# Optimization experiments

Measured on AMD Instinct MI355X. Metric: run time of the kernel, lower is better.

The kernel has to match this reference:

```python
import jax, jax.numpy as jnp
import numpy as np

B, T, D, H = 2, 2048, 1024, 16
HD = D // H  # head_dim = 64


def setup_inputs() -> dict:
    key = jax.random.key(0)
    ks = jax.random.split(key, 5)
    s = 0.02
    return {
        "x": jax.random.normal(ks[0], (B, T, D), dtype=jnp.float32),
        "Wqkv": jax.random.normal(ks[1], (3 * D, D), dtype=jnp.float32) * s,
        "bqkv": jax.random.normal(ks[2], (3 * D,), dtype=jnp.float32) * s,
        "Wproj": jax.random.normal(ks[3], (D, D), dtype=jnp.float32) * s,
        "bproj": jax.random.normal(ks[4], (D,), dtype=jnp.float32) * s,
    }


def reference(x, Wqkv, bqkv, Wproj, bproj):
    b, t, d = x.shape
    qkv = x @ Wqkv.T + bqkv                      # [B,T,3D]
    q, k, v = jnp.split(qkv, 3, axis=-1)
    # [B,T,D] -> [B,H,T,HD]
    def to_heads(u):
        return u.reshape(b, t, H, HD).transpose(0, 2, 1, 3)
    q, k, v = to_heads(q), to_heads(k), to_heads(v)
    scale = 1.0 / jnp.sqrt(jnp.float32(HD))
    attn = jnp.einsum("bhqd,bhkd->bhqk", q, k) * scale   # [B,H,T,T]
    causal = jnp.tril(jnp.ones((t, t), dtype=bool))
    attn = jnp.where(causal[None, None, :, :], attn, -jnp.inf)
    attn = jax.nn.softmax(attn, axis=-1)
    scores = jnp.einsum("bhqk,bhkd->bhqd", attn, v)       # [B,H,T,HD]
    scores = scores.transpose(0, 2, 1, 3).reshape(b, t, d)
    return scores @ Wproj.T + bproj
```

## Files before the change

kernel.cpp:

```cpp
#include <hip/hip_runtime.h>

typedef __bf16 bf16_8 __attribute__((ext_vector_type(8)));
typedef __bf16 bf16_4 __attribute__((ext_vector_type(4)));
typedef float  f32_4  __attribute__((ext_vector_type(4)));
typedef short  s16x4  __attribute__((ext_vector_type(4)));

typedef __attribute__((address_space(1))) const void* as1_cvp;
typedef __attribute__((address_space(3))) void*       as3_vp;

__device__ __forceinline__ void load16_to_lds(const void* g, void* l) {
    __builtin_amdgcn_global_load_lds((as1_cvp)g, (as3_vp)l, 16, 0, 0);
}

__device__ __forceinline__ f32_4 mfma16x16x16(bf16_4 a, bf16_4 b, f32_4 c) {
#if __has_builtin(__builtin_amdgcn_mfma_f32_16x16x16_bf16)
    return __builtin_amdgcn_mfma_f32_16x16x16_bf16(a, b, c, 0, 0, 0);
#else
    return __builtin_amdgcn_mfma_f32_16x16x16bf16_1k(
        __builtin_bit_cast(s16x4, a), __builtin_bit_cast(s16x4, b), c, 0, 0, 0);
#endif
}

__global__ __launch_bounds__(256) void cvt_all(
    const float* __restrict__ a, const float* __restrict__ b,
    const float* __restrict__ c, __bf16* __restrict__ out,
    int na4, int nb4, int nc4)
{
    int i = blockIdx.x * 256 + threadIdx.x;
    if (i >= na4 + nb4 + nc4) return;
    float4 f;
    if (i < na4)            f = ((const float4*)a)[i];
    else if (i < na4 + nb4) f = ((const float4*)b)[i - na4];
    else                    f = ((const float4*)c)[i - na4 - nb4];
    bf16_4 v = { (__bf16)f.x, (__bf16)f.y, (__bf16)f.z, (__bf16)f.w };
    ((bf16_4*)out)[i] = v;
}

#define BM 128

template<int OUT_BF16, int BN_, int QKV>
__global__ __launch_bounds__(256) void gemm_bt(
    const __bf16* __restrict__ A,
    const __bf16* __restrict__ B,
    const float*  __restrict__ bias,
    __bf16* __restrict__ Cb, float* __restrict__ Cf,
    __bf16* __restrict__ Vtb,
    int M, int N, int K, int ldc)
{
    constexpr int NT   = BN_ / 32;
    constexpr int CSTR = BN_ + (OUT_BF16 ? 8 : 4);
    __shared__ __align__(16) char smem[34816];
    __bf16* As = (__bf16*)smem;
    __bf16* Bs = (__bf16*)(smem + 16384);

    const int tid  = threadIdx.x;
    const int wave = tid >> 6;
    const int lane = tid & 63;
    const int wm = wave >> 1, wn = wave & 1;
    const int quad = lane >> 4, l16 = lane & 15;
    const int bm = blockIdx.y * BM, bn = blockIdx.x * BN_;

    const int r0 = tid >> 2;
    const int cf = ((tid & 3) ^ (r0 & 3)) * 8;

    f32_4 acc[4][NT];
    #pragma unroll
    for (int i = 0; i < 4; ++i)
        #pragma unroll
        for (int j = 0; j < NT; ++j)
            acc[i][j] = f32_4{0.f, 0.f, 0.f, 0.f};

    const int NIT = K >> 5;

    {
        #pragma unroll
        for (int p = 0; p < 2; ++p)
            load16_to_lds(A + (size_t)(bm + p * 64 + r0) * K + cf,
                          &As[(p * 64 + wave * 16) * 32]);
        #pragma unroll
        for (int p = 0; p < BN_ / 64; ++p)
            load16_to_lds(B + (size_t)(bn + p * 64 + r0) * K + cf,
                          &Bs[(p * 64 + wave * 16) * 32]);
    }

    for (int j = 0; j < NIT; ++j) {
        const int cur = j & 1, nxt = cur ^ 1;
        __syncthreads();

        if (j + 1 < NIT) {
            const int k0 = (j + 1) * 32;
            #pragma unroll
            for (int p = 0; p < 2; ++p)
                load16_to_lds(A + (size_t)(bm + p * 64 + r0) * K + k0 + cf,
                              &As[nxt * 4096 + (p * 64 + wave * 16) * 32]);
            #pragma unroll
            for (int p = 0; p < BN_ / 64; ++p)
                load16_to_lds(B + (size_t)(bn + p * 64 + r0) * K + k0 + cf,
                              &Bs[nxt * (BN_ * 32) + (p * 64 + wave * 16) * 32]);
        }

        const int sl = ((quad ^ (l16 & 3)) << 3);
        bf16_8 af[4], bfr[NT];
        #pragma unroll
        for (int mt = 0; mt < 4; ++mt)
            af[mt] = *(const bf16_8*)&As[cur * 4096 + (wm * 64 + mt * 16 + l16) * 32 + sl];
        #pragma unroll
        for (int nt = 0; nt < NT; ++nt)
            bfr[nt] = *(const bf16_8*)&Bs[cur * (BN_ * 32) + (wn * (BN_/2) + nt * 16 + l16) * 32 + sl];
        #pragma unroll
        for (int mt = 0; mt < 4; ++mt)
            #pragma unroll
            for (int nt = 0; nt < NT; ++nt)
                acc[mt][nt] = __builtin_amdgcn_mfma_f32_16x16x32_bf16(
                    af[mt], bfr[nt], acc[mt][nt], 0, 0, 0);
    }

    __syncthreads();

    if (QKV && bn >= 2048) {
        constexpr int VSTR = 136;
        __bf16* Cs = (__bf16*)smem;
        const int b_ = bm >> 11;
        const int t0 = bm & 2047;
        #pragma unroll
        for (int nt = 0; nt < NT; ++nt) {
            int col = wn * (BN_/2) + nt * 16 + l16;
            float bv = bias ? bias[bn + col] : 0.f;
            #pragma unroll
            for (int mt = 0; mt < 4; ++mt) {
                bf16_4 ov;
                #pragma unroll
                for (int r = 0; r < 4; ++r)
                    ov[r] = (__bf16)(acc[mt][nt][r] + bv);
                *(bf16_4*)&Cs[col * VSTR + wm * 64 + mt * 16 + quad * 4] = ov;
            }
        }
        __syncthreads();
        const int rr = tid >> 1, hh = tid & 1;
        #pragma unroll
        for (int c = 0; c < 8; ++c) {
            bf16_8 v = *(const bf16_8*)&Cs[rr * VSTR + (hh * 8 + c) * 8];
            *(bf16_8*)(Vtb + ((size_t)b_ * 1024 + (bn - 2048) + rr) * 2048
                       + t0 + (hh * 8 + c) * 8) = v;
        }
        return;
    }

    if (OUT_BF16) {
        __bf16* Cs = (__bf16*)smem;
        #pragma unroll
        for (int mt = 0; mt < 4; ++mt)
            #pragma unroll
            for (int nt = 0; nt < NT; ++nt) {
                int col = wn * (BN_/2) + nt * 16 + l16;
                float bv = bias ? bias[bn + col] : 0.f;
                #pragma unroll
                for (int r = 0; r < 4; ++r)
                    Cs[(wm * 64 + mt * 16 + quad * 4 + r) * CSTR + col] =
                        (__bf16)(acc[mt][nt][r] + bv);
            }
        __syncthreads();
        const int rr = tid >> 4, cc = (tid & 15) * 8;
        #pragma unroll
        for (int p = 0; p < 8; ++p) {
            int row = p * 16 + rr;
            bf16_8 v = *(const bf16_8*)&Cs[row * CSTR + cc];
            *(bf16_8*)(Cb + (size_t)(bm + row) * ldc + bn + cc) = v;
        }
    } else {
        float* Cs = (float*)smem;
        #pragma unroll
        for (int mt = 0; mt < 4; ++mt)
            #pragma unroll
            for (int nt = 0; nt < NT; ++nt) {
                int col = wn * (BN_/2) + nt * 16 + l16;
                float bv = bias ? bias[bn + col] : 0.f;
                #pragma unroll
                for (int r = 0; r < 4; ++r)
                    Cs[(wm * 64 + mt * 16 + quad * 4 + r) * CSTR + col] =
                        acc[mt][nt][r] + bv;
            }
        __syncthreads();
        const int rr = tid >> 4, cc = (tid & 15) * 4;
        #pragma unroll
        for (int p = 0; p < 8; ++p) {
            int row = p * 16 + rr;
            float4 v = *(const float4*)&Cs[row * CSTR + cc];
            *(float4*)(Cf + (size_t)(bm + row) * ldc + bn + cc) = v;
        }
    }
}

__global__ __launch_bounds__(512, 4) void attn_kernel(
    const __bf16* __restrict__ qk, const __bf16* __restrict__ vt,
    __bf16* __restrict__ out)
{
    constexpr int T = 2048;
    __shared__ __align__(16) char pool[35328];
    __bf16* Ks = (__bf16*)pool;
    __bf16* Vt = (__bf16*)(pool + 16384);
    float*  Om = (float*)pool;
    float*  Lm = (float*)(pool + 34816);

    const int tid  = threadIdx.x;
    const int wave = tid >> 6;
    const int lane = tid & 63;
    const int wg = wave >> 2, wq = wave & 3;
    const int quad = lane >> 4, l16 = lane & 15;

    const int fid  = blockIdx.x;
    const int xcd  = fid & 7;
    const int half = fid >> 8;
    const int w    = (fid >> 3) & 31;
    const int qt   = half ? (7 - (w >> 2)) : ((w >> 2) + 8);
    const int bh   = xcd * 4 + (w & 3);
    const int b = bh >> 4, h = bh & 15;
    const int jmax = 2 * qt + 1;

    const size_t rowbase = (size_t)b * T;
    const __bf16* Kbase = qk + 1024 + h * 64;
    const __bf16* Vbase = vt + (size_t)bh * 64 * 2048;

    const int srow = tid >> 3;
    const int sch  = tid & 7;
    const int schf = sch ^ (srow & 7);

    bf16_8 aq[2][2];
    #pragma unroll
    for (int mt = 0; mt < 2; ++mt) {
        const __bf16* qrow =
            qk + (rowbase + qt * 128 + wq * 32 + mt * 16 + l16) * 2048 + h * 64;
        aq[mt][0] = *(const bf16_8*)(qrow + quad * 8);
        aq[mt][1] = *(const bf16_8*)(qrow + 32 + quad * 8);
        #pragma unroll
        for (int u = 0; u < 8; ++u) {
            aq[mt][0][u] = (__bf16)((float)aq[mt][0][u] * 0.125f);
            aq[mt][1][u] = (__bf16)((float)aq[mt][1][u] * 0.125f);
        }
    }

    load16_to_lds(Kbase + (rowbase + srow) * 2048 + schf * 8, &Ks[wave * 512]);
    load16_to_lds(Vbase + (size_t)srow * 2048 + schf * 8,     &Vt[wave * 512]);

    float l_i[2] = {0.f, 0.f};
    f32_4 O[2][4];
    #pragma unroll
    for (int mt = 0; mt < 2; ++mt)
        #pragma unroll
        for (int dt = 0; dt < 4; ++dt) O[mt][dt] = f32_4{0.f, 0.f, 0.f, 0.f};

    for (int j = 0; j <= jmax; ++j) {
        const int cur = j & 1, nxt = cur ^ 1;
        __syncthreads();

        if (j < jmax) {
            const int jn = j + 1;
            load16_to_lds(Kbase + (rowbase + jn * 64 + srow) * 2048 + schf * 8,
                          &Ks[nxt * 4096 + wave * 512]);
            load16_to_lds(Vbase + (size_t)srow * 2048 + jn * 64 + schf * 8,
                          &Vt[nxt * 4096 + wave * 512]);
        }

        f32_4 S[2][2];
        #pragma unroll
        for (int nt = 0; nt < 2; ++nt) {
            int rk = wg * 32 + nt * 16 + l16;
            int rx = rk & 7;
            bf16_8 kb0 = *(const bf16_8*)&Ks[cur * 4096 + rk * 64 + ((quad ^ rx) << 3)];
            bf16_8 kb1 = *(const bf16_8*)&Ks[cur * 4096 + rk * 64 + (((quad + 4) ^ rx) << 3)];
            #pragma unroll
            for (int mt = 0; mt < 2; ++mt) {
                f32_4 zz = {0.f, 0.f, 0.f, 0.f};
                zz = __builtin_amdgcn_mfma_f32_16x16x32_bf16(kb0, aq[mt][0], zz, 0, 0, 0);
                zz = __builtin_amdgcn_mfma_f32_16x16x32_bf16(kb1, aq[mt][1], zz, 0, 0, 0);
                S[mt][nt] = zz;
            }
        }

        const bool diag = (j >= 2 * qt);
        bf16_4 bp[2][2];
        #pragma unroll
        for (int mt = 0; mt < 2; ++mt) {
            int qg = qt * 128 + wq * 32 + mt * 16 + l16;
            #pragma unroll
            for (int nt = 0; nt < 2; ++nt) {
                #pragma unroll
                for (int rr = 0; rr < 4; ++rr) {
                    float p = __expf(S[mt][nt][rr]);
                    if (diag) {
                        int key = j * 64 + wg * 32 + nt * 16 + quad * 4 + rr;
                        if (key > qg) p = 0.f;
                    }
                    l_i[mt] += p;
                    bp[mt][nt][rr] = (__bf16)p;
                }
            }
        }

        #pragma unroll
        for (int dt = 0; dt < 4; ++dt) {
            int d = dt * 16 + l16;
            int dsw = d & 7;
            #pragma unroll
            for (int nt = 0; nt < 2; ++nt) {
                int chv = (wg * 4 + nt * 2 + (quad >> 1)) ^ dsw;
                bf16_4 vaf = *(const bf16_4*)&Vt[cur * 4096 + d * 64 + chv * 8 + (quad & 1) * 4];
                #pragma unroll
                for (int mt = 0; mt < 2; ++mt)
                    O[mt][dt] = mfma16x16x16(vaf, bp[mt][nt], O[mt][dt]);
            }
        }
    }

    float lw[2];
    #pragma unroll
    for (int mt = 0; mt < 2; ++mt) {
        float v = l_i[mt];
        v += __shfl_xor(v, 16, 64);
        v += __shfl_xor(v, 32, 64);
        lw[mt] = v;
    }
    __syncthreads();
    if (wg == 1) {
        #pragma unroll
        for (int mt = 0; mt < 2; ++mt) {
            #pragma unroll
            for (int dt = 0; dt < 4; ++dt)
                *(f32_4*)&Om[(wq * 32 + mt * 16 + l16) * 68 + dt * 16 + quad * 4] = O[mt][dt];
            if (quad == 0) Lm[wq * 32 + mt * 16 + l16] = lw[mt];
        }
    }
    __syncthreads();
    if (wg == 0) {
        #pragma unroll
        for (int mt = 0; mt < 2; ++mt) {
            float inv = 1.f / (lw[mt] + Lm[wq * 32 + mt * 16 + l16]);
            int q = qt * 128 + wq * 32 + mt * 16 + l16;
            #pragma unroll
            for (int dt = 0; dt < 4; ++dt) {
                f32_4 o2 = *(const f32_4*)&Om[(wq * 32 + mt * 16 + l16) * 68 + dt * 16 + quad * 4];
                bf16_4 ov;
                #pragma unroll
                for (int rr = 0; rr < 4; ++rr)
                    ov[rr] = (__bf16)((O[mt][dt][rr] + o2[rr]) * inv);
                *(bf16_4*)(out + (rowbase + q) * 1024 + h * 64 + dt * 16 + quad * 4) = ov;
            }
        }
    }
}

extern "C" void kernel_launch(void* const* d_in, const int* in_sizes, int n_in,
                              void* d_out, int out_size, void* d_ws, size_t ws_size,
                              hipStream_t stream)
{
    constexpr int Bc = 2, Tc = 2048, Dc = 1024;
    constexpr int M  = Bc * Tc;
    constexpr int N1 = 3 * Dc;

    const float* x     = (const float*)d_in[0];
    const float* Wqkv  = (const float*)d_in[1];
    const float* bqkv  = (const float*)d_in[2];
    const float* Wproj = (const float*)d_in[3];
    const float* bproj = (const float*)d_in[4];
    float* outp = (float*)d_out;

    __bf16* xb     = (__bf16*)d_ws;
    __bf16* wqkvb  = xb     + (size_t)M * Dc;
    __bf16* wprojb = wqkvb  + (size_t)N1 * Dc;
    __bf16* qkb    = wprojb + (size_t)Dc * Dc;
    __bf16* vtb    = qkb    + (size_t)M * 2048;
    __bf16* attnb  = vtb    + (size_t)Bc * 1024 * 2048;

    {
        int na4 = M * Dc / 4, nb4 = N1 * Dc / 4, nc4 = Dc * Dc / 4;
        int n4 = na4 + nb4 + nc4;
        cvt_all<<<(n4 + 255) / 256, 256, 0, stream>>>(x, Wqkv, Wproj, xb, na4, nb4, nc4);
    }

    gemm_bt<1, 128, 1><<<dim3(N1 / 128, M / BM), 256, 0, stream>>>(
        xb, wqkvb, bqkv, qkb, nullptr, vtb, M, N1, Dc, 2048);

    attn_kernel<<<dim3(512), 512, 0, stream>>>(qkb, vtb, attnb);

    gemm_bt<0, 64, 0><<<dim3(Dc / 64, M / BM), 256, 0, stream>>>(
        attnb, wprojb, bproj, nullptr, outp, nullptr, M, Dc, Dc, Dc);
}
```

Baseline: 170.6 us.

## Enlarge attention KV tiles, give each block two balanced query tiles

The attention kernel now loads 128-key K/V tiles per iteration and each wave handles 64 query rows across 4 key groups. Each block processes a pair of query tiles (z+8 and 7-z) in sequence, which balances causal work, and the grid is halved to 256 blocks. The cross-wave reduction becomes a two-stage LDS reduce with a swizzled layout. The GEMM LDS swizzle pattern is also changed to reduce bank conflicts. Risks: LDS doubles to about 66KB, occupancy drops (launch bounds go from 4 to 2), and the accumulators use more registers.

```diff
diff --git a/kernel.cpp b/kernel.cpp
--- a/kernel.cpp
+++ b/kernel.cpp
@@ -61,7 +61,7 @@
     const int bm = blockIdx.y * BM, bn = blockIdx.x * BN_;
 
     const int r0 = tid >> 2;
-    const int cf = ((tid & 3) ^ (r0 & 3)) * 8;
+    const int cf = ((tid & 3) ^ ((tid >> 3) & 3)) * 8;
 
     f32_4 acc[4][NT];
     #pragma unroll
@@ -99,7 +99,7 @@
                               &Bs[nxt * (BN_ * 32) + (p * 64 + wave * 16) * 32]);
         }
 
-        const int sl = ((quad ^ (l16 & 3)) << 3);
+        const int sl = ((quad ^ ((l16 >> 1) & 3)) << 3);
         bf16_8 af[4], bfr[NT];
         #pragma unroll
         for (int mt = 0; mt < 4; ++mt)
@@ -191,161 +191,199 @@
     }
 }
 
-__global__ __launch_bounds__(512, 4) void attn_kernel(
+__global__ __launch_bounds__(512, 2) void attn_kernel(
     const __bf16* __restrict__ qk, const __bf16* __restrict__ vt,
     __bf16* __restrict__ out)
 {
     constexpr int T = 2048;
-    __shared__ __align__(16) char pool[35328];
+    __shared__ __align__(16) char pool[67584];
     __bf16* Ks = (__bf16*)pool;
-    __bf16* Vt = (__bf16*)(pool + 16384);
+    __bf16* Vt = (__bf16*)(pool + 32768);
     float*  Om = (float*)pool;
-    float*  Lm = (float*)(pool + 34816);
+    float*  Lm = (float*)(pool + 65536);
 
     const int tid  = threadIdx.x;
     const int wave = tid >> 6;
     const int lane = tid & 63;
-    const int wg = wave >> 2, wq = wave & 3;
+    const int wq = wave >> 2;
+    const int wg = wave & 3;
     const int quad = lane >> 4, l16 = lane & 15;
 
-    const int fid  = blockIdx.x;
-    const int xcd  = fid & 7;
-    const int half = fid >> 8;
-    const int w    = (fid >> 3) & 31;
-    const int qt   = half ? (7 - (w >> 2)) : ((w >> 2) + 8);
-    const int bh   = xcd * 4 + (w & 3);
+    const int fid = blockIdx.x;
+    const int xcd = fid & 7;
+    const int w   = fid >> 3;
+    const int bh  = xcd * 4 + (w & 3);
+    const int z   = w >> 2;
     const int b = bh >> 4, h = bh & 15;
-    const int jmax = 2 * qt + 1;
 
     const size_t rowbase = (size_t)b * T;
     const __bf16* Kbase = qk + 1024 + h * 64;
     const __bf16* Vbase = vt + (size_t)bh * 64 * 2048;
 
-    const int srow = tid >> 3;
-    const int sch  = tid & 7;
-    const int schf = sch ^ (srow & 7);
-
-    bf16_8 aq[2][2];
+    const int krow = tid >> 3, kch = tid & 7;
+    const int vd   = tid >> 4, vch = tid & 15;
+
     #pragma unroll
-    for (int mt = 0; mt < 2; ++mt) {
-        const __bf16* qrow =
-            qk + (rowbase + qt * 128 + wq * 32 + mt * 16 + l16) * 2048 + h * 64;
-        aq[mt][0] = *(const bf16_8*)(qrow + quad * 8);
-        aq[mt][1] = *(const bf16_8*)(qrow + 32 + quad * 8);
-        #pragma unroll
-        for (int u = 0; u < 8; ++u) {
-            aq[mt][0][u] = (__bf16)((float)aq[mt][0][u] * 0.125f);
-            aq[mt][1][u] = (__bf16)((float)aq[mt][1][u] * 0.125f);
-        }
-    }
-
-    load16_to_lds(Kbase + (rowbase + srow) * 2048 + schf * 8, &Ks[wave * 512]);
-    load16_to_lds(Vbase + (size_t)srow * 2048 + schf * 8,     &Vt[wave * 512]);
-
-    float l_i[2] = {0.f, 0.f};
-    f32_4 O[2][4];
-    #pragma unroll
-    for (int mt = 0; mt < 2; ++mt)
-        #pragma unroll
-        for (int dt = 0; dt < 4; ++dt) O[mt][dt] = f32_4{0.f, 0.f, 0.f, 0.f};
-
-    for (int j = 0; j <= jmax; ++j) {
-        const int cur = j & 1, nxt = cur ^ 1;
-        __syncthreads();
-
-        if (j < jmax) {
-            const int jn = j + 1;
-            load16_to_lds(Kbase + (rowbase + jn * 64 + srow) * 2048 + schf * 8,
-                          &Ks[nxt * 4096 + wave * 512]);
-            load16_to_lds(Vbase + (size_t)srow * 2048 + jn * 64 + schf * 8,
-                          &Vt[nxt * 4096 + wave * 512]);
-        }
-
-        f32_4 S[2][2];
-        #pragma unroll
-        for (int nt = 0; nt < 2; ++nt) {
-            int rk = wg * 32 + nt * 16 + l16;
-            int rx = rk & 7;
-            bf16_8 kb0 = *(const bf16_8*)&Ks[cur * 4096 + rk * 64 + ((quad ^ rx) << 3)];
-            bf16_8 kb1 = *(const bf16_8*)&Ks[cur * 4096 + rk * 64 + (((quad + 4) ^ rx) << 3)];
-            #pragma unroll
-            for (int mt = 0; mt < 2; ++mt) {
-                f32_4 zz = {0.f, 0.f, 0.f, 0.f};
-                zz = __builtin_amdgcn_mfma_f32_16x16x32_bf16(kb0, aq[mt][0], zz, 0, 0, 0);
-                zz = __builtin_amdgcn_mfma_f32_16x16x32_bf16(kb1, aq[mt][1], zz, 0, 0, 0);
-                S[mt][nt] = zz;
-            }
-        }
-
-        const bool diag = (j >= 2 * qt);
-        bf16_4 bp[2][2];
-        #pragma unroll
-        for (int mt = 0; mt < 2; ++mt) {
-            int qg = qt * 128 + wq * 32 + mt * 16 + l16;
+    for (int tile = 0; tile < 2; ++tile) {
+        const int qt   = tile ? (7 - z) : (z + 8);
+        const int jmax = qt;
+
+        bf16_8 aq[4][2];
+        #pragma unroll
+        for (int m = 0; m < 4; ++m) {
+            const __bf16* qrow =
+                qk + (rowbase + qt * 128 + wq * 64 + m * 16 + l16) * 2048 + h * 64;
+            aq[m][0] = *(const bf16_8*)(qrow + quad * 8);
+            aq[m][1] = *(const bf16_8*)(qrow + 32 + quad * 8);
+            #pragma unroll
+            for (int u = 0; u < 8; ++u) {
+                aq[m][0][u] = (__bf16)((float)aq[m][0][u] * 0.125f);
+                aq[m][1][u] = (__bf16)((float)aq[m][1][u] * 0.125f);
+            }
+        }
+
+        #pragma unroll
+        for (int p = 0; p < 2; ++p) {
+            int r = p * 64 + krow;
+            load16_to_lds(Kbase + (rowbase + r) * 2048 + ((kch ^ (r & 7)) * 8),
+                          &Ks[(p * 64 + wave * 8) * 64]);
+            int d = p * 32 + vd;
+            load16_to_lds(Vbase + (size_t)d * 2048 + ((vch ^ (d & 7)) * 8),
+                          &Vt[(p * 32 + wave * 4) * 128]);
+        }
+
+        float l_i[4] = {0.f, 0.f, 0.f, 0.f};
+        f32_4 O[4][4];
+        #pragma unroll
+        for (int m = 0; m < 4; ++m)
+            #pragma unroll
+            for (int dt = 0; dt < 4; ++dt) O[m][dt] = f32_4{0.f, 0.f, 0.f, 0.f};
+
+        for (int j = 0; j <= jmax; ++j) {
+            const int cur = j & 1, nxt = cur ^ 1;
+            __syncthreads();
+
+            if (j < jmax) {
+                const int jn = j + 1;
+                #pragma unroll
+                for (int p = 0; p < 2; ++p) {
+                    int r = p * 64 + krow;
+                    load16_to_lds(Kbase + (rowbase + jn * 128 + r) * 2048 + ((kch ^ (r & 7)) * 8),
+                                  &Ks[nxt * 8192 + (p * 64 + wave * 8) * 64]);
+                    int d = p * 32 + vd;
+                    load16_to_lds(Vbase + (size_t)d * 2048 + jn * 128 + ((vch ^ (d & 7)) * 8),
+                                  &Vt[nxt * 8192 + (p * 32 + wave * 4) * 128]);
+                }
+            }
+
+            const bool diag = (j == qt);
+            bf16_4 bp[4][2];
             #pragma unroll
             for (int nt = 0; nt < 2; ++nt) {
-                #pragma unroll
-                for (int rr = 0; rr < 4; ++rr) {
-                    float p = __expf(S[mt][nt][rr]);
-                    if (diag) {
-                        int key = j * 64 + wg * 32 + nt * 16 + quad * 4 + rr;
-                        if (key > qg) p = 0.f;
+                int rk = wg * 32 + nt * 16 + l16;
+                int rx = rk & 7;
+                bf16_8 kb0 = *(const bf16_8*)&Ks[cur * 8192 + rk * 64 + ((quad ^ rx) << 3)];
+                bf16_8 kb1 = *(const bf16_8*)&Ks[cur * 8192 + rk * 64 + (((quad + 4) ^ rx) << 3)];
+                #pragma unroll
+                for (int m = 0; m < 4; ++m) {
+                    f32_4 zz = {0.f, 0.f, 0.f, 0.f};
+                    zz = __builtin_amdgcn_mfma_f32_16x16x32_bf16(kb0, aq[m][0], zz, 0, 0, 0);
+                    zz = __builtin_amdgcn_mfma_f32_16x16x32_bf16(kb1, aq[m][1], zz, 0, 0, 0);
+                    int qg = qt * 128 + wq * 64 + m * 16 + l16;
+                    #pragma unroll
+                    for (int rr = 0; rr < 4; ++rr) {
+                        float p = __expf(zz[rr]);
+                        if (diag) {
+                            int key = j * 128 + wg * 32 + nt * 16 + quad * 4 + rr;
+                            if (key > qg) p = 0.f;
+                        }
+                        l_i[m] += p;
+                        bp[m][nt][rr] = (__bf16)p;
                     }
-                    l_i[mt] += p;
-                    bp[mt][nt][rr] = (__bf16)p;
                 }
             }
-        }
-
-        #pragma unroll
-        for (int dt = 0; dt < 4; ++dt) {
-            int d = dt * 16 + l16;
-            int dsw = d & 7;
-            #pragma unroll
-            for (int nt = 0; nt < 2; ++nt) {
-                int chv = (wg * 4 + nt * 2 + (quad >> 1)) ^ dsw;
-                bf16_4 vaf = *(const bf16_4*)&Vt[cur * 4096 + d * 64 + chv * 8 + (quad & 1) * 4];
-                #pragma unroll
-                for (int mt = 0; mt < 2; ++mt)
-                    O[mt][dt] = mfma16x16x16(vaf, bp[mt][nt], O[mt][dt]);
-            }
-        }
-    }
-
-    float lw[2];
-    #pragma unroll
-    for (int mt = 0; mt < 2; ++mt) {
-        float v = l_i[mt];
-        v += __shfl_xor(v, 16, 64);
-        v += __shfl_xor(v, 32, 64);
-        lw[mt] = v;
-    }
-    __syncthreads();
-    if (wg == 1) {
-        #pragma unroll
-        for (int mt = 0; mt < 2; ++mt) {
-            #pragma unroll
-            for (int dt = 0; dt < 4; ++dt)
-                *(f32_4*)&Om[(wq * 32 + mt * 16 + l16) * 68 + dt * 16 + quad * 4] = O[mt][dt];
-            if (quad == 0) Lm[wq * 32 + mt * 16 + l16] = lw[mt];
-        }
-    }
-    __syncthreads();
-    if (wg == 0) {
-        #pragma unroll
-        for (int mt = 0; mt < 2; ++mt) {
-            float inv = 1.f / (lw[mt] + Lm[wq * 32 + mt * 16 + l16]);
-            int q = qt * 128 + wq * 32 + mt * 16 + l16;
+
             #pragma unroll
             for (int dt = 0; dt < 4; ++dt) {
-                f32_4 o2 = *(const f32_4*)&Om[(wq * 32 + mt * 16 + l16) * 68 + dt * 16 + quad * 4];
-                bf16_4 ov;
-                #pragma unroll
-                for (int rr = 0; rr < 4; ++rr)
-                    ov[rr] = (__bf16)((O[mt][dt][rr] + o2[rr]) * inv);
-                *(bf16_4*)(out + (rowbase + q) * 1024 + h * 64 + dt * 16 + quad * 4) = ov;
-            }
-        }
+                int d = dt * 16 + l16;
+                int dsw = d & 7;
+                #pragma unroll
+                for (int nt = 0; nt < 2; ++nt) {
+                    int c = wg * 4 + nt * 2 + (quad >> 1);
+                    bf16_4 vaf = *(const bf16_4*)&Vt[cur * 8192 + d * 128
+                                                     + ((c ^ dsw) << 3) + (quad & 1) * 4];
+                    #pragma unroll
+                    for (int m = 0; m < 4; ++m)
+                        O[m][dt] = mfma16x16x16(vaf, bp[m][nt], O[m][dt]);
+                }
+            }
+        }
+
+        float lw[4];
+        #pragma unroll
+        for (int m = 0; m < 4; ++m) {
+            float v = l_i[m];
+            v += __shfl_xor(v, 16, 64);
+            v += __shfl_xor(v, 32, 64);
+            lw[m] = v;
+        }
+        __syncthreads();
+        if (wg >= 2) {
+            float* slot = Om + (wq * 2 + (wg - 2)) * 4096;
+            #pragma unroll
+            for (int m = 0; m < 4; ++m)
+                #pragma unroll
+                for (int dt = 0; dt < 4; ++dt)
+                    *(f32_4*)&slot[(m * 16 + l16) * 64 + (((dt * 4 + quad) ^ (l16 & 7)) << 2)]
+                        = O[m][dt];
+        }
+        if (quad == 0)
+            #pragma unroll
+            for (int m = 0; m < 4; ++m)
+                Lm[(wq * 4 + wg) * 64 + m * 16 + l16] = lw[m];
+        __syncthreads();
+        if (wg < 2) {
+            float* slot = Om + (wq * 2 + wg) * 4096;
+            #pragma unroll
+            for (int m = 0; m < 4; ++m)
+                #pragma unroll
+                for (int dt = 0; dt < 4; ++dt)
+                    O[m][dt] += *(const f32_4*)&slot[(m * 16 + l16) * 64
+                                 + (((dt * 4 + quad) ^ (l16 & 7)) << 2)];
+        }
+        if (wg == 1) {
+            float* slot = Om + (wq * 2 + 1) * 4096;
+            #pragma unroll
+            for (int m = 0; m < 4; ++m)
+                #pragma unroll
+                for (int dt = 0; dt < 4; ++dt)
+                    *(f32_4*)&slot[(m * 16 + l16) * 64 + (((dt * 4 + quad) ^ (l16 & 7)) << 2)]
+                        = O[m][dt];
+        }
+        __syncthreads();
+        if (wg == 0) {
+            float* slot = Om + (wq * 2 + 1) * 4096;
+            #pragma unroll
+            for (int m = 0; m < 4; ++m) {
+                float ls = lw[m];
+                #pragma unroll
+                for (int g = 1; g < 4; ++g)
+                    ls += Lm[(wq * 4 + g) * 64 + m * 16 + l16];
+                float inv = 1.f / ls;
+                int q = qt * 128 + wq * 64 + m * 16 + l16;
+                #pragma unroll
+                for (int dt = 0; dt < 4; ++dt) {
+                    f32_4 o2 = *(const f32_4*)&slot[(m * 16 + l16) * 64
+                                 + (((dt * 4 + quad) ^ (l16 & 7)) << 2)];
+                    bf16_4 ov;
+                    #pragma unroll
+                    for (int rr = 0; rr < 4; ++rr)
+                        ov[rr] = (__bf16)((O[m][dt][rr] + o2[rr]) * inv);
+                    *(bf16_4*)(out + (rowbase + q) * 1024 + h * 64 + dt * 16 + quad * 4) = ov;
+                }
+            }
+        }
+        __syncthreads();
     }
 }
 
@@ -380,7 +418,7 @@
     gemm_bt<1, 128, 1><<<dim3(N1 / 128, M / BM), 256, 0, stream>>>(
         xb, wqkvb, bqkv, qkb, nullptr, vtb, M, N1, Dc, 2048);
 
-    attn_kernel<<<dim3(512), 512, 0, stream>>>(qkb, vtb, attnb);
+    attn_kernel<<<dim3(256), 512, 0, stream>>>(qkb, vtb, attnb);
 
     gemm_bt<0, 64, 0><<<dim3(Dc / 64, M / BM), 256, 0, stream>>>(
         attnb, wprojb, bproj, nullptr, outp, nullptr, M, Dc, Dc, Dc);
```

Result: slower. 176.6 us (+3.5%).
